# Optimization experiments

Measured on AMD Instinct MI355X. Metric: run time of the kernel, lower is better.

Reference implementation:

```python
import jax, jax.numpy as jnp
import numpy as np

B, T, NH, HS = 2, 2048, 16, 64
C = NH * HS
V_SHIFT = 1          # value shift; queries start at position V_SHIFT
EXP_SCALE = 10.0     # exp_param_scale
KB_UP = 5.0          # kernel_beta_upbound


def setup_inputs() -> dict:
    key = jax.random.key(0)
    ks = jax.random.split(key, 8)
    s = 0.02
    return {
        "x": jax.random.normal(ks[0], (B, T, C), jnp.float32),
        # leaky-average key path: linear proj + per-head decay coefficient
        "W_la": jax.random.normal(ks[1], (C, C), jnp.float32) * s,
        "la_coef": jax.random.uniform(ks[2], (NH,), jnp.float32, 0.1, 0.9),
        "kernel_beta": jnp.ones((NH,), jnp.float32) / EXP_SCALE,
        "value_beta": jnp.ones((NH,), jnp.float32) * (-0.5) / EXP_SCALE,
        # value featurizer (lowrlinearconv): linear + per-head mixing coef
        "W_v": jax.random.normal(ks[3], (C, C), jnp.float32) * s,
        "v_coef": jax.random.uniform(ks[4], (NH,), jnp.float32, 0.0, 1.0),
        "W_proj": jax.random.normal(ks[5], (C, C), jnp.float32) * s,
    }


def reference(x, W_la, la_coef, kernel_beta, value_beta, W_v, v_coef, W_proj):
    B_, T_, C_ = x.shape
    # ---- keys: leaky average (per-head EMA recurrence) of linear projection ----
    xl = (x @ W_la).reshape(B_, T_, NH, HS)          # (B,T,nh,hs)
    alpha = la_coef.reshape(NH, 1)                   # per-head decay

    def step(carry, xt):  # carry,xt: (B,nh,hs)
        new = alpha * carry + (1.0 - alpha) * xt
        return new, new

    _, kt = jax.lax.scan(step, jnp.zeros((B_, NH, HS), x.dtype),
                         jnp.swapaxes(xl, 0, 1))    # (T,B,nh,hs)
    k = jnp.transpose(kt, (1, 2, 0, 3))              # (B,nh,T,hs)
    k = k / jnp.linalg.norm(k, axis=-1, keepdims=True)
    kb = jnp.exp(jnp.minimum(kernel_beta * EXP_SCALE, KB_UP)).reshape(1, NH, 1, 1)
    k = k * kb

    # ---- values: lowrlinearconv featurizer (shift=1, kernel=2) + L2 norm ----
    xv = (x @ W_v).reshape(B_, T_, NH, HS).transpose(0, 2, 1, 3)   # (B,nh,T,hs)
    xv_sh = jnp.concatenate([xv[:, :, 1:], jnp.zeros_like(xv[:, :, :1])], axis=2)
    c = v_coef.reshape(1, NH, 1, 1)
    v = xv_sh * (1.0 - c) + xv * c
    v = v / jnp.linalg.norm(v, axis=-1, keepdims=True)
    v = v * jnp.exp(value_beta * EXP_SCALE).reshape(1, NH, 1, 1)

    # ---- shifted-causal masked SDPA (scale=1); queries are positions >= V_SHIFT ----
    q = k[:, :, V_SHIFT:]                            # (B,nh,T-1,hs)
    scores = jnp.einsum('bhqd,bhkd->bhqk', q, k)
    qpos = jnp.arange(V_SHIFT, T_)[:, None]
    kpos = jnp.arange(T_)[None, :]
    mask = kpos < qpos                               # key j visible iff j < query position
    scores = jnp.where(mask, scores, -jnp.inf)
    att = jax.nn.softmax(scores, axis=-1)
    y_att = jnp.einsum('bhqk,bhkd->bhqd', att, v)
    y = jnp.concatenate([jnp.zeros((B_, NH, V_SHIFT, HS), x.dtype), y_att], axis=2)
    y = jnp.transpose(y, (0, 2, 1, 3)).reshape(B_, T_, C_)
    return y @ W_proj                                # dropouts are eval-mode identity
```

## Files before the change

kernel.cpp:

```cpp
#include <hip/hip_runtime.h>
#include <hip/hip_bf16.h>

#define B_  2
#define T_  2048
#define NH_ 16
#define HS_ 64
#define C_  1024
#define SCL_ 128
#define SCN_ (T_ / SCL_)
#define NT_  (T_ / 64)
#define TEL_ 4096

typedef __attribute__((ext_vector_type(8))) short bf16x8;
typedef __attribute__((ext_vector_type(4))) float f32x4;

__device__ inline int pack_bf16(float a, float b) {
  union { __hip_bfloat16 h; unsigned short u; } ua, ub;
  ua.h = __float2bfloat16(a);
  ub.h = __float2bfloat16(b);
  return (int)(((unsigned)ub.u << 16) | (unsigned)ua.u);
}

__device__ inline void gl_lds16(const __hip_bfloat16* g, __hip_bfloat16* l) {
  __builtin_amdgcn_global_load_lds(
      (const __attribute__((address_space(1))) unsigned int*)g,
      (__attribute__((address_space(3))) unsigned int*)l, 16, 0, 0);
}

__global__ __launch_bounds__(256) void cvt_bf16_kernel(const float* __restrict__ in,
                                                       __hip_bfloat16* __restrict__ out) {
  const int i = (blockIdx.x * 256 + threadIdx.x) * 8;
  const float4 a = *reinterpret_cast<const float4*>(in + i);
  const float4 b = *reinterpret_cast<const float4*>(in + i + 4);
  union { int s[4]; int4 v; } u;
  u.s[0] = pack_bf16(a.x, a.y);
  u.s[1] = pack_bf16(a.z, a.w);
  u.s[2] = pack_bf16(b.x, b.y);
  u.s[3] = pack_bf16(b.z, b.w);
  *reinterpret_cast<int4*>(out + i) = u.v;
}

__global__ __launch_bounds__(256) void cvtT_all_kernel(const float* __restrict__ W_la,
                                                       const float* __restrict__ W_v,
                                                       const float* __restrict__ W_proj,
                                                       __hip_bfloat16* __restrict__ Wcat,
                                                       __hip_bfloat16* __restrict__ WprojT) {
  __shared__ __hip_bfloat16 tile[64][66];
  const int z = blockIdx.z;
  const float* W = (z == 0) ? W_la : (z == 1) ? W_v : W_proj;
  __hip_bfloat16* WT = (z == 2) ? WprojT : Wcat + (size_t)z * C_ * C_;
  const int w = threadIdx.x >> 6, l = threadIdx.x & 63;
  const int n0 = blockIdx.x * 64, k0 = blockIdx.y * 64;
#pragma unroll
  for (int r = 0; r < 16; ++r) {
    const int k = k0 + w * 16 + r;
    tile[w * 16 + r][l] = __float2bfloat16(W[(size_t)k * C_ + n0 + l]);
  }
  __syncthreads();
#pragma unroll
  for (int r = 0; r < 16; ++r) {
    const int nn = w * 16 + r;
    WT[(size_t)(n0 + nn) * C_ + k0 + l] = tile[l][nn];
  }
}

__global__ __launch_bounds__(256) void gemm_in_kernel(const __hip_bfloat16* __restrict__ A,
                                                      const __hip_bfloat16* __restrict__ BT,
                                                      float* __restrict__ C0,
                                                      float* __restrict__ C1) {
  __shared__ __hip_bfloat16 As[128 * 32];
  __shared__ __hip_bfloat16 Bs[128 * 32];
  const int tid = threadIdx.x;
  const int m0 = blockIdx.y * 128, n0 = blockIdx.x * 128;
  const int w = tid >> 6, l = tid & 63;
  const int n = l & 15, kg = l >> 4;
  const int m0w = (w & 1) * 64, n0w = (w >> 1) * 64;

  const int r0 = tid >> 2, o0 = (tid & 3) * 8;
  const __hip_bfloat16* ag0 = A + (size_t)(m0 + r0) * C_ + o0;
  const __hip_bfloat16* ag1 = A + (size_t)(m0 + 64 + r0) * C_ + o0;
  const __hip_bfloat16* bg0 = BT + (size_t)(n0 + r0) * C_ + o0;
  const __hip_bfloat16* bg1 = BT + (size_t)(n0 + 64 + r0) * C_ + o0;
  __hip_bfloat16* al0 = As + tid * 8;
  __hip_bfloat16* al1 = As + (256 + tid) * 8;
  __hip_bfloat16* bl0 = Bs + tid * 8;
  __hip_bfloat16* bl1 = Bs + (256 + tid) * 8;

  f32x4 acc[4][4];
#pragma unroll
  for (int i = 0; i < 4; ++i)
#pragma unroll
    for (int j = 0; j < 4; ++j) acc[i][j] = f32x4{0.f, 0.f, 0.f, 0.f};

  for (int k0 = 0; k0 < C_; k0 += 32) {
    gl_lds16(ag0 + k0, al0);
    gl_lds16(ag1 + k0, al1);
    gl_lds16(bg0 + k0, bl0);
    gl_lds16(bg1 + k0, bl1);
    __syncthreads();
    bf16x8 af[4], bf[4];
#pragma unroll
    for (int ms = 0; ms < 4; ++ms)
      af[ms] = *reinterpret_cast<const bf16x8*>(As + (m0w + ms * 16 + n) * 32 + kg * 8);
#pragma unroll
    for (int ns = 0; ns < 4; ++ns)
      bf[ns] = *reinterpret_cast<const bf16x8*>(Bs + (n0w + ns * 16 + n) * 32 + kg * 8);
#pragma unroll
    for (int ms = 0; ms < 4; ++ms)
#pragma unroll
      for (int ns = 0; ns < 4; ++ns)
        acc[ms][ns] = __builtin_amdgcn_mfma_f32_16x16x32_bf16(af[ms], bf[ns], acc[ms][ns], 0, 0, 0);
    __syncthreads();
  }

  float* Cb = (n0 < C_) ? C0 : C1;
  const int nc = (n0 < C_) ? n0 : n0 - C_;
#pragma unroll
  for (int ms = 0; ms < 4; ++ms) {
#pragma unroll
    for (int r = 0; r < 4; ++r) {
      const int row = m0 + m0w + ms * 16 + kg * 4 + r;
      float* cp = Cb + (size_t)row * C_ + nc + n0w + n;
#pragma unroll
      for (int ns = 0; ns < 4; ++ns) cp[ns * 16] = acc[ms][ns][r];
    }
  }
}

__global__ __launch_bounds__(256) void gemm_proj_kernel(const __hip_bfloat16* __restrict__ A,
                                                        const __hip_bfloat16* __restrict__ BT,
                                                        float* __restrict__ Cout) {
  __shared__ __hip_bfloat16 As[64 * 32];
  __shared__ __hip_bfloat16 Bs[128 * 32];
  const int tid = threadIdx.x;
  const int m0 = blockIdx.y * 64, n0 = blockIdx.x * 128;
  const int w = tid >> 6, l = tid & 63;
  const int n = l & 15, kg = l >> 4;

  const int r0 = tid >> 2, o0 = (tid & 3) * 8;
  const __hip_bfloat16* ag = A + (size_t)(m0 + r0) * C_ + o0;
  const __hip_bfloat16* bg0 = BT + (size_t)(n0 + r0) * C_ + o0;
  const __hip_bfloat16* bg1 = BT + (size_t)(n0 + 64 + r0) * C_ + o0;
  __hip_bfloat16* al = As + tid * 8;
  __hip_bfloat16* bl0 = Bs + tid * 8;
  __hip_bfloat16* bl1 = Bs + (256 + tid) * 8;

  f32x4 acc[4][2];
#pragma unroll
  for (int i = 0; i < 4; ++i)
#pragma unroll
    for (int j = 0; j < 2; ++j) acc[i][j] = f32x4{0.f, 0.f, 0.f, 0.f};

  for (int k0 = 0; k0 < C_; k0 += 32) {
    gl_lds16(ag + k0, al);
    gl_lds16(bg0 + k0, bl0);
    gl_lds16(bg1 + k0, bl1);
    __syncthreads();
    bf16x8 af[4], bf[2];
#pragma unroll
    for (int ms = 0; ms < 4; ++ms)
      af[ms] = *reinterpret_cast<const bf16x8*>(As + (ms * 16 + n) * 32 + kg * 8);
#pragma unroll
    for (int ns = 0; ns < 2; ++ns)
      bf[ns] = *reinterpret_cast<const bf16x8*>(Bs + (w * 32 + ns * 16 + n) * 32 + kg * 8);
#pragma unroll
    for (int ms = 0; ms < 4; ++ms)
#pragma unroll
      for (int ns = 0; ns < 2; ++ns)
        acc[ms][ns] = __builtin_amdgcn_mfma_f32_16x16x32_bf16(af[ms], bf[ns], acc[ms][ns], 0, 0, 0);
    __syncthreads();
  }

#pragma unroll
  for (int ms = 0; ms < 4; ++ms) {
#pragma unroll
    for (int r = 0; r < 4; ++r) {
      const int row = m0 + ms * 16 + kg * 4 + r;
      float* cp = Cout + (size_t)row * C_ + n0 + w * 32 + n;
#pragma unroll
      for (int ns = 0; ns < 2; ++ns) cp[ns * 16] = acc[ms][ns][r];
    }
  }
}

__global__ __launch_bounds__(256) void ema_local_kernel(const float* __restrict__ xl,
                                                        float* __restrict__ loc,
                                                        float* __restrict__ carr,
                                                        const float* __restrict__ la_coef) {
  const int c = blockIdx.x % SCN_;
  const int bh = blockIdx.x / SCN_;
  const int b = bh / NH_, h = bh % NH_;
  const int tid = threadIdx.x;
  const int t0 = c * SCL_;
  __shared__ float buf[SCL_ * HS_];

  const float alpha = la_coef[h];
  const float onema = 1.0f - alpha;
  const float4* src4 = reinterpret_cast<const float4*>(xl + (size_t)b * T_ * C_ + h * HS_);

  float4* buf4 = reinterpret_cast<float4*>(buf);
#pragma unroll
  for (int i = 0; i < (SCL_ * HS_ / 4) / 256; ++i) {
    const int idx = tid + i * 256;
    const int tt = idx >> 4, d4 = idx & 15;
    buf4[tt * 16 + d4] = src4[(size_t)(t0 + tt) * (C_ / 4) + d4];
  }
  __syncthreads();
  if (tid < 64) {
    const int d = tid;
    float c2 = 0.0f;
#pragma unroll 8
    for (int tt = 0; tt < SCL_; ++tt) {
      c2 = alpha * c2 + onema * buf[tt * HS_ + d];
      buf[tt * HS_ + d] = c2;
    }
    carr[(size_t)(bh * SCN_ + c) * HS_ + d] = c2;
  }
  __syncthreads();
  float4* dst4 = reinterpret_cast<float4*>(loc + ((size_t)bh * T_ + t0) * HS_);
#pragma unroll
  for (int i = 0; i < (SCL_ * HS_ / 4) / 256; ++i) dst4[tid + i * 256] = buf4[tid + i * 256];
}

__global__ __launch_bounds__(256) void ema_fix_norm_kernel(const float* __restrict__ loc,
                                                           const float* __restrict__ carr,
                                                           __hip_bfloat16* __restrict__ kb16,
                                                           const float* __restrict__ la_coef,
                                                           const float* __restrict__ kernel_beta) {
  const int c = blockIdx.x % SCN_;
  const int bh = blockIdx.x / SCN_;
  const int h = bh % NH_;
  const int w = threadIdx.x >> 6, l = threadIdx.x & 63;

  const float alpha = la_coef[h];
  const float aL = __powf(alpha, (float)SCL_);
  const float kbs = expf(fminf(kernel_beta[h] * 10.0f, 5.0f));

  float A = 0.0f;
  for (int cc = 0; cc < c; ++cc) A = aL * A + carr[(size_t)(bh * SCN_ + cc) * HS_ + l];

  const float* lp = loc + ((size_t)bh * T_ + c * SCL_ + w * 32) * HS_ + l;
  __hip_bfloat16* kt = kb16 + (size_t)bh * NT_ * TEL_;
  const int g = l >> 3, j = l & 7;

  float s = __powf(alpha, (float)(w * 32 + 1));
  for (int rr = 0; rr < 32; ++rr) {
    const int t = c * SCL_ + w * 32 + rr;
    float val = lp[rr * HS_] + s * A;
    float ss = val * val;
#pragma unroll
    for (int m = 32; m; m >>= 1) ss += __shfl_xor(ss, m);
    const int tile = t >> 6, key = t & 63;
    kt[(size_t)tile * TEL_ + (g * 64 + key) * 8 + j] = __float2bfloat16(val * (kbs / sqrtf(ss)));
    s *= alpha;
  }
}

__global__ __launch_bounds__(256) void vprep_kernel(const float* __restrict__ xv,
                                                    __hip_bfloat16* __restrict__ vt,
                                                    const float* __restrict__ value_beta,
                                                    const float* __restrict__ v_coef) {
  const int tc = blockIdx.x % NT_;
  const int bh = blockIdx.x / NT_;
  const int h = bh % NH_, b = bh / NH_;
  const int t0 = tc * 64;
  const int w = threadIdx.x >> 6, l = threadIdx.x & 63;
  __shared__ __hip_bfloat16 tile[64][66];

  const float c = v_coef[h];
  const float vb = expf(value_beta[h] * 10.0f);

  for (int r = 0; r < 16; ++r) {
    const int tl = w * 16 + r;
    const int t = t0 + tl;
    const float* base = xv + ((size_t)b * T_ + t) * C_ + h * HS_ + l;
    const float cur = base[0];
    const float nxt = (t + 1 < T_) ? base[C_] : 0.0f;
    float val = nxt * (1.0f - c) + cur * c;
    float ssum = val * val;
#pragma unroll
    for (int m = 32; m; m >>= 1) ssum += __shfl_xor(ssum, m);
    tile[tl][l] = __float2bfloat16(val * (vb / sqrtf(ssum)));
  }
  __syncthreads();
  __hip_bfloat16* vtb = vt + (size_t)(bh * NT_ + tc) * TEL_;
  const int kk = l >> 3, j = l & 7;
  for (int rr = 0; rr < 16; ++rr) {
    const int hs = w * 16 + rr;
    vtb[(kk * 64 + hs) * 8 + j] = tile[l][hs];
  }
}

__global__ __launch_bounds__(256) void attn_mfma_kernel(
    const __hip_bfloat16* __restrict__ kb,
    const __hip_bfloat16* __restrict__ vt,
    __hip_bfloat16* __restrict__ y) {
  __shared__ __hip_bfloat16 Ks[TEL_];
  __shared__ __hip_bfloat16 Vs[TEL_];
  __shared__ __hip_bfloat16 Ps[4][16 * 68];

  const int id = (int)blockIdx.x;
  const int xcd = id & 7;
  const int s = id >> 3;
  const int bh = xcd + 8 * (s & 3);
  const int qt = (NT_ - 1) - (s >> 2);
  const int b = bh / NH_, h = bh % NH_;
  const int q0 = qt * 64;
  const int w = threadIdx.x >> 6;
  const int l = threadIdx.x & 63;
  const int n = l & 15;
  const int kg = l >> 4;
  const int qq = w * 16 + n;
  const int query = q0 + qq;
  const int lo = l * 8;
  const int tb = bh * NT_;

  bf16x8 qf0, qf1;
  {
    const __hip_bfloat16* qtile = kb + (size_t)(tb + qt) * TEL_;
    qf0 = *reinterpret_cast<const bf16x8*>(qtile + (kg * 64 + qq) * 8);
    qf1 = *reinterpret_cast<const bf16x8*>(qtile + ((kg + 4) * 64 + qq) * 8);
  }

  f32x4 accO[4];
#pragma unroll
  for (int i = 0; i < 4; ++i) accO[i] = f32x4{0.f, 0.f, 0.f, 0.f};
  float l_acc = 0.0f;

  __hip_bfloat16* Pw = Ps[w];
  int* Pwi = reinterpret_cast<int*>(Pw);

  for (int jt = 0; jt <= qt; ++jt) {
    __syncthreads();
    {
      const size_t tg = (size_t)(tb + jt) * TEL_;
      gl_lds16(kb + tg + w * 1024 + lo, &Ks[w * 1024 + lo]);
      gl_lds16(kb + tg + w * 1024 + 512 + lo, &Ks[w * 1024 + 512 + lo]);
      gl_lds16(vt + tg + w * 1024 + lo, &Vs[w * 1024 + lo]);
      gl_lds16(vt + tg + w * 1024 + 512 + lo, &Vs[w * 1024 + 512 + lo]);
    }
    __syncthreads();

    const bool diag = (jt == qt);

    f32x4 accS[4];
#pragma unroll
    for (int ms = 0; ms < 4; ++ms) {
      bf16x8 a0 = *reinterpret_cast<const bf16x8*>(Ks + (kg * 64 + ms * 16 + n) * 8);
      bf16x8 a1 = *reinterpret_cast<const bf16x8*>(Ks + ((kg + 4) * 64 + ms * 16 + n) * 8);
      f32x4 z{0.f, 0.f, 0.f, 0.f};
      z = __builtin_amdgcn_mfma_f32_16x16x32_bf16(a0, qf0, z, 0, 0, 0);
      accS[ms] = __builtin_amdgcn_mfma_f32_16x16x32_bf16(a1, qf1, z, 0, 0, 0);
    }

    float lsum = 0.0f;
#pragma unroll
    for (int ms = 0; ms < 4; ++ms) {
      const int kbase = ms * 16 + kg * 4;
      float p[4];
#pragma unroll
      for (int r = 0; r < 4; ++r) {
        const float e = __expf(accS[ms][r]);
        p[r] = (!diag || (kbase + r < qq)) ? e : 0.0f;
        lsum += p[r];
      }
      const int po = n * 34 + ms * 8 + kg * 2;
      Pwi[po] = pack_bf16(p[0], p[1]);
      Pwi[po + 1] = pack_bf16(p[2], p[3]);
    }
    lsum += __shfl_xor(lsum, 16);
    lsum += __shfl_xor(lsum, 32);
    l_acc += lsum;

#pragma unroll
    for (int ks = 0; ks < 2; ++ks) {
      union { ushort4 u[2]; bf16x8 v; } pr;
      const __hip_bfloat16* pp = Pw + n * 68 + ks * 32 + kg * 8;
      pr.u[0] = *reinterpret_cast<const ushort4*>(pp);
      pr.u[1] = *reinterpret_cast<const ushort4*>(pp + 4);
#pragma unroll
      for (int mo = 0; mo < 4; ++mo) {
        bf16x8 av = *reinterpret_cast<const bf16x8*>(Vs + ((ks * 4 + kg) * 64 + mo * 16 + n) * 8);
        accO[mo] = __builtin_amdgcn_mfma_f32_16x16x32_bf16(av, pr.v, accO[mo], 0, 0, 0);
      }
    }
  }

  const float inv = (query == 0) ? 0.0f : 1.0f / l_acc;
  __hip_bfloat16* yb = y + ((size_t)b * T_ + query) * C_ + h * HS_;
#pragma unroll
  for (int mo = 0; mo < 4; ++mo) {
    int2 pkd;
    pkd.x = pack_bf16(accO[mo][0] * inv, accO[mo][1] * inv);
    pkd.y = pack_bf16(accO[mo][2] * inv, accO[mo][3] * inv);
    *reinterpret_cast<int2*>(yb + mo * 16 + kg * 4) = pkd;
  }
}

extern "C" void kernel_launch(void* const* d_in, const int* in_sizes, int n_in,
                              void* d_out, int out_size, void* d_ws, size_t ws_size,
                              hipStream_t stream) {
  const float* x           = (const float*)d_in[0];
  const float* W_la        = (const float*)d_in[1];
  const float* la_coef     = (const float*)d_in[2];
  const float* kernel_beta = (const float*)d_in[3];
  const float* value_beta  = (const float*)d_in[4];
  const float* W_v         = (const float*)d_in[5];
  const float* v_coef      = (const float*)d_in[6];
  const float* W_proj      = (const float*)d_in[7];
  float* out = (float*)d_out;

  char* wsb = (char*)d_ws;
  const size_t MB = 1024u * 1024u;
  __hip_bfloat16* x16    = (__hip_bfloat16*)(wsb);
  __hip_bfloat16* Wcat   = (__hip_bfloat16*)(wsb + 8 * MB);
  __hip_bfloat16* WprojT = (__hip_bfloat16*)(wsb + 12 * MB);
  float* carr            = (float*)(wsb + 14 * MB);
  float* xl              = (float*)(wsb + 16 * MB);
  float* xv              = (float*)(wsb + 32 * MB);
  __hip_bfloat16* kb16   = (__hip_bfloat16*)(wsb + 48 * MB);
  __hip_bfloat16* vt16   = (__hip_bfloat16*)(wsb + 56 * MB);
  float* loc             = xv;
  __hip_bfloat16* y16    = (__hip_bfloat16*)(wsb + 16 * MB);
  (void)ws_size; (void)in_sizes; (void)n_in; (void)out_size;

  const int M = B_ * T_;

  cvt_bf16_kernel<<<dim3((M * C_) / 2048), dim3(256), 0, stream>>>(x, x16);
  cvtT_all_kernel<<<dim3(C_ / 64, C_ / 64, 3), dim3(256), 0, stream>>>(W_la, W_v, W_proj, Wcat, WprojT);

  gemm_in_kernel<<<dim3(2 * C_ / 128, M / 128), dim3(256), 0, stream>>>(x16, Wcat, xl, xv);
  vprep_kernel<<<dim3(B_ * NH_ * NT_), dim3(256), 0, stream>>>(xv, vt16, value_beta, v_coef);
  ema_local_kernel<<<dim3(B_ * NH_ * SCN_), dim3(256), 0, stream>>>(xl, loc, carr, la_coef);
  ema_fix_norm_kernel<<<dim3(B_ * NH_ * SCN_), dim3(256), 0, stream>>>(loc, carr, kb16, la_coef, kernel_beta);
  attn_mfma_kernel<<<dim3(8 * 128), dim3(256), 0, stream>>>(kb16, vt16, y16);
  gemm_proj_kernel<<<dim3(C_ / 128, M / 64), dim3(256), 0, stream>>>(y16, WprojT, out);
}
```

Baseline: 220.2 us.

## Double-buffer K/V tiles in attention with async prefetch and MFMA priority

The attention kernel now keeps two LDS buffers each for K and V. It issues the global-to-LDS loads for tile jt+1 before computing on tile jt, using manual s_waitcnt vmcnt and raw barriers in place of __syncthreads. This overlaps the load latency with the MFMA and softmax work. It also raises wave priority around the MFMA sections. In exchange, LDS use roughly doubles, which may lower occupancy, and correctness now depends on the hand-written vmcnt counts and barrier placement.

```diff
diff --git a/kernel.cpp b/kernel.cpp
--- a/kernel.cpp
+++ b/kernel.cpp
@@ -295,8 +295,8 @@
     const __hip_bfloat16* __restrict__ kb,
     const __hip_bfloat16* __restrict__ vt,
     __hip_bfloat16* __restrict__ y) {
-  __shared__ __hip_bfloat16 Ks[TEL_];
-  __shared__ __hip_bfloat16 Vs[TEL_];
+  __shared__ __hip_bfloat16 Ks[2 * TEL_];
+  __shared__ __hip_bfloat16 Vs[2 * TEL_];
   __shared__ __hip_bfloat16 Ps[4][16 * 68];
 
   const int id = (int)blockIdx.x;
@@ -314,6 +314,7 @@
   const int query = q0 + qq;
   const int lo = l * 8;
   const int tb = bh * NT_;
+  const int so = w * 1024 + lo;
 
   bf16x8 qf0, qf1;
   {
@@ -330,28 +331,49 @@
   __hip_bfloat16* Pw = Ps[w];
   int* Pwi = reinterpret_cast<int*>(Pw);
 
+  {
+    const size_t tg = (size_t)tb * TEL_;
+    gl_lds16(kb + tg + so, Ks + so);
+    gl_lds16(kb + tg + so + 512, Ks + so + 512);
+    gl_lds16(vt + tg + so, Vs + so);
+    gl_lds16(vt + tg + so + 512, Vs + so + 512);
+  }
+
+  int cur = 0;
   for (int jt = 0; jt <= qt; ++jt) {
-    __syncthreads();
-    {
-      const size_t tg = (size_t)(tb + jt) * TEL_;
-      gl_lds16(kb + tg + w * 1024 + lo, &Ks[w * 1024 + lo]);
-      gl_lds16(kb + tg + w * 1024 + 512 + lo, &Ks[w * 1024 + 512 + lo]);
-      gl_lds16(vt + tg + w * 1024 + lo, &Vs[w * 1024 + lo]);
-      gl_lds16(vt + tg + w * 1024 + 512 + lo, &Vs[w * 1024 + 512 + lo]);
-    }
-    __syncthreads();
+    asm volatile("" ::: "memory");
+    __builtin_amdgcn_s_barrier();
+    asm volatile("" ::: "memory");
+
+    if (jt < qt) {
+      const size_t tg = (size_t)(tb + jt + 1) * TEL_;
+      const int bo = (cur ^ 1) * TEL_ + so;
+      gl_lds16(kb + tg + so, Ks + bo);
+      gl_lds16(kb + tg + so + 512, Ks + bo + 512);
+      gl_lds16(vt + tg + so, Vs + bo);
+      gl_lds16(vt + tg + so + 512, Vs + bo + 512);
+      asm volatile("s_waitcnt vmcnt(4)" ::: "memory");
+    } else {
+      asm volatile("s_waitcnt vmcnt(0)" ::: "memory");
+    }
+    __builtin_amdgcn_s_barrier();
+    asm volatile("" ::: "memory");
 
     const bool diag = (jt == qt);
+    const __hip_bfloat16* Kc = Ks + cur * TEL_;
+    const __hip_bfloat16* Vc = Vs + cur * TEL_;
 
     f32x4 accS[4];
+    __builtin_amdgcn_s_setprio(1);
 #pragma unroll
     for (int ms = 0; ms < 4; ++ms) {
-      bf16x8 a0 = *reinterpret_cast<const bf16x8*>(Ks + (kg * 64 + ms * 16 + n) * 8);
-      bf16x8 a1 = *reinterpret_cast<const bf16x8*>(Ks + ((kg + 4) * 64 + ms * 16 + n) * 8);
+      bf16x8 a0 = *reinterpret_cast<const bf16x8*>(Kc + (kg * 64 + ms * 16 + n) * 8);
+      bf16x8 a1 = *reinterpret_cast<const bf16x8*>(Kc + ((kg + 4) * 64 + ms * 16 + n) * 8);
       f32x4 z{0.f, 0.f, 0.f, 0.f};
       z = __builtin_amdgcn_mfma_f32_16x16x32_bf16(a0, qf0, z, 0, 0, 0);
       accS[ms] = __builtin_amdgcn_mfma_f32_16x16x32_bf16(a1, qf1, z, 0, 0, 0);
     }
+    __builtin_amdgcn_s_setprio(0);
 
     float lsum = 0.0f;
 #pragma unroll
@@ -372,6 +394,7 @@
     lsum += __shfl_xor(lsum, 32);
     l_acc += lsum;
 
+    __builtin_amdgcn_s_setprio(1);
 #pragma unroll
     for (int ks = 0; ks < 2; ++ks) {
       union { ushort4 u[2]; bf16x8 v; } pr;
@@ -380,10 +403,13 @@
       pr.u[1] = *reinterpret_cast<const ushort4*>(pp + 4);
 #pragma unroll
       for (int mo = 0; mo < 4; ++mo) {
-        bf16x8 av = *reinterpret_cast<const bf16x8*>(Vs + ((ks * 4 + kg) * 64 + mo * 16 + n) * 8);
+        bf16x8 av = *reinterpret_cast<const bf16x8*>(Vc + ((ks * 4 + kg) * 64 + mo * 16 + n) * 8);
         accO[mo] = __builtin_amdgcn_mfma_f32_16x16x32_bf16(av, pr.v, accO[mo], 0, 0, 0);
       }
     }
+    __builtin_amdgcn_s_setprio(0);
+
+    cur ^= 1;
   }
 
   const float inv = (query == 0) ? 0.0f : 1.0f / l_acc;
```

Result: no change. 222.7 us (+1.1%).
